# Kernel tuning notes

Hardware: AMD Instinct MI355X
Metric: run time of the kernel (lower is better)

The kernel has to match this reference:

```python
import jax, jax.numpy as jnp
import numpy as np

H = 256
W = 256
CHUNK = 100  # faces per rasterizer scan step


def _cross2(o, p, q):
    # 2D cross product of (p-o) x (q-o); broadcasts over leading dims
    return (p[..., 0] - o[..., 0]) * (q[..., 1] - o[..., 1]) - (p[..., 1] - o[..., 1]) * (q[..., 0] - o[..., 0])


def transform(verts, K, Rt):
    # verts [B,V,3] -> pixel coords [B,V,3] = (x_pix, y_pix, z_cam)
    v_cam = jnp.einsum('bij,bnj->bni', Rt[:, :, :3], verts) + Rt[:, None, :, 3]
    v_proj = jnp.einsum('bij,bnj->bni', K, v_cam)
    z = v_cam[..., 2:3]
    return jnp.concatenate([v_proj[..., :2] / z, z], axis=-1)


def _pixel_centers(h, w, dtype):
    px = jnp.arange(w, dtype=dtype) + 0.5
    py = jnp.arange(h, dtype=dtype) + 0.5
    gx, gy = jnp.meshgrid(px, py, indexing='xy')  # [h,w]
    return gx, gy


def rasterize(v_pix, vi, h, w):
    # z-buffered triangle rasterization -> index image [B,h,w] (int32, -1 = bg)
    B = v_pix.shape[0]
    Fc = vi.shape[0]
    gx, gy = _pixel_centers(h, w, v_pix.dtype)
    pix = jnp.stack([gx.ravel(), gy.ravel()], axis=-1)  # [HW,2]
    face_ids = jnp.arange(Fc, dtype=jnp.int32).reshape(-1, CHUNK)
    inf = jnp.asarray(jnp.inf, v_pix.dtype)

    def step(carry, fids):
        best_z, best_i = carry
        tri = vi[fids]                      # [C,3]
        p = v_pix[:, tri]                   # [B,C,3,3]
        a, b, c = p[:, :, 0], p[:, :, 1], p[:, :, 2]
        area = _cross2(a[..., :2], b[..., :2], c[..., :2])  # [B,C]
        pixb = pix[None, None]              # [1,1,HW,2]
        w0 = _cross2(b[..., None, :2], c[..., None, :2], pixb)  # [B,C,HW]
        w1 = _cross2(c[..., None, :2], a[..., None, :2], pixb)
        w2 = _cross2(a[..., None, :2], b[..., None, :2], pixb)
        s = jnp.sign(area)[..., None]
        nz = jnp.abs(area)[..., None] > 1e-8
        inside = (w0 * s >= 0) & (w1 * s >= 0) & (w2 * s >= 0) & nz
        za, zb, zc = a[..., 2:3], b[..., 2:3], c[..., 2:3]
        valid = inside & (za > 0) & (zb > 0) & (zc > 0)
        ar = jnp.where(jnp.abs(area) > 1e-8, area, 1.0)[..., None]
        invz = (w0 / ar) / za + (w1 / ar) / zb + (w2 / ar) / zc  # persp-correct 1/z
        z = jnp.where(valid & (invz > 0), 1.0 / jnp.maximum(invz, 1e-12), inf)
        cz = z.min(axis=1)                  # [B,HW]
        ci = z.argmin(axis=1)
        cf = fids[ci]
        upd = cz < best_z
        return (jnp.where(upd, cz, best_z), jnp.where(upd, cf, best_i)), None

    init = (jnp.full((B, h * w), jnp.inf, v_pix.dtype), jnp.full((B, h * w), -1, jnp.int32))
    (_, bi), _ = jax.lax.scan(step, init, face_ids)
    return bi.reshape(B, h, w)


def render(v_pix, vi, index_img):
    # depth [B,h,w] and perspective-correct barycentrics [B,3,h,w]
    B, h, w = index_img.shape
    tri = vi[jnp.clip(index_img, 0)]                 # [B,h,w,3]
    p = jax.vmap(lambda v, t: v[t])(v_pix, tri)      # [B,h,w,3,3]
    gx, gy = _pixel_centers(h, w, v_pix.dtype)
    pt = jnp.stack([gx, gy], axis=-1)[None]          # [1,h,w,2]
    a, b, c = p[..., 0, :], p[..., 1, :], p[..., 2, :]
    w0 = _cross2(b[..., :2], c[..., :2], pt)
    w1 = _cross2(c[..., :2], a[..., :2], pt)
    w2 = _cross2(a[..., :2], b[..., :2], pt)
    area = w0 + w1 + w2
    ar = jnp.where(jnp.abs(area) > 1e-8, area, 1.0)
    f0 = (w0 / ar) / jnp.maximum(a[..., 2], 1e-8)
    f1 = (w1 / ar) / jnp.maximum(b[..., 2], 1e-8)
    f2 = (w2 / ar) / jnp.maximum(c[..., 2], 1e-8)
    invz = f0 + f1 + f2
    invz_s = jnp.where(jnp.abs(invz) > 1e-12, invz, 1.0)
    depth = 1.0 / invz_s
    bary = jnp.stack([f0, f1, f2], axis=-1) / invz_s[..., None]  # [B,h,w,3]
    m = index_img != -1
    depth_img = jnp.where(m, depth, 0.0)
    bary_img = jnp.where(m[..., None], bary, 0.0).transpose(0, 3, 1, 2)  # [B,3,h,w]
    return depth_img, bary_img


def interpolate(attr, vti, index_img, bary_img):
    # attr [B,N,D], bary_img [B,3,h,w] -> [B,D,h,w]
    tri = vti[jnp.clip(index_img, 0)]                # [B,h,w,3]
    av = jax.vmap(lambda a, t: a[t])(attr, tri)      # [B,h,w,3,D]
    return jnp.einsum('bhwkd,bkhw->bdhw', av, bary_img)


def grid_sample_bilinear(tex, grid):
    # tex [B,C,Ht,Wt], grid [B,h,w,2] in [-1,1]; align_corners=False, zero pad
    B, C, Ht, Wt = tex.shape
    x = (grid[..., 0] + 1.0) * Wt / 2.0 - 0.5
    y = (grid[..., 1] + 1.0) * Ht / 2.0 - 0.5
    x0 = jnp.floor(x)
    y0 = jnp.floor(y)
    wx = (x - x0)[:, None]
    wy = (y - y0)[:, None]
    x0i = x0.astype(jnp.int32)
    y0i = y0.astype(jnp.int32)

    def gat(ix, iy):
        valid = (ix >= 0) & (ix < Wt) & (iy >= 0) & (iy < Ht)
        ixc = jnp.clip(ix, 0, Wt - 1)
        iyc = jnp.clip(iy, 0, Ht - 1)
        v = jax.vmap(lambda t, yy, xx: t[:, yy, xx])(tex, iyc, ixc)  # [B,C,h,w]
        return v * valid[:, None].astype(tex.dtype)

    return (gat(x0i, y0i) * (1 - wx) * (1 - wy)
            + gat(x0i + 1, y0i) * wx * (1 - wy)
            + gat(x0i, y0i + 1) * (1 - wx) * wy
            + gat(x0i + 1, y0i + 1) * wx * wy)


def reference(verts, tex, K, Rt, vt, vi, vti):
    v_pix = transform(verts, K, Rt)
    index_img = jax.lax.stop_gradient(rasterize(v_pix, vi, H, W))
    depth_img, bary_img = render(v_pix, vi, index_img)
    B = verts.shape[0]
    vt_attr = jnp.broadcast_to((vt * 2.0 - 1.0)[None], (B,) + vt.shape)
    vt_img = interpolate(vt_attr, vti, index_img, bary_img)    # [B,2,H,W]
    mask = (index_img != -1)[:, None].astype(tex.dtype)
    img = grid_sample_bilinear(tex, vt_img.transpose(0, 2, 3, 1)) * mask
    # edge_grad_estimator is identity in the forward pass
    return img, depth_img, v_pix, vt_img, index_img, bary_img, mask


def setup_inputs() -> dict:
    key = jax.random.key(0)
    ks = jax.random.split(key, 6)
    B, V, Fc, Nvt = 2, 5000, 10000, 5000
    xy = jax.random.uniform(ks[0], (B, V, 2), minval=-1.5, maxval=1.5)
    z = jax.random.uniform(ks[1], (B, V, 1), minval=2.0, maxval=4.0)
    verts = jnp.concatenate([xy, z], axis=-1)
    tex = jax.random.uniform(ks[2], (B, 3, 1024, 1024), dtype=jnp.float32)
    K = jnp.broadcast_to(jnp.array([[256., 0., 128.], [0., 256., 128.], [0., 0., 1.]], dtype=jnp.float32), (B, 3, 3))
    Rt = jnp.broadcast_to(jnp.concatenate([jnp.eye(3, dtype=jnp.float32), jnp.zeros((3, 1), jnp.float32)], axis=1), (B, 3, 4))
    vt = jax.random.uniform(ks[3], (Nvt, 2), dtype=jnp.float32)
    vi = jax.random.randint(ks[4], (Fc, 3), 0, V).astype(jnp.int32)
    vti = jax.random.randint(ks[5], (Fc, 3), 0, Nvt).astype(jnp.int32)
    return {"verts": verts, "tex": tex, "K": K, "Rt": Rt, "vt": vt, "vi": vi, "vti": vti}
```

## Files before the change

kernel.cpp:

```cpp
#include <hip/hip_runtime.h>
#include <cmath>

#define H_ 256
#define W_ 256
#define SEG 4
#define NB 256
#define NBAND (H_ / 4)
#define ILV 4
#define REC_STRIDE 24
#define INITKEY 0x7f800000FFFFFFFFull

__device__ inline unsigned fkey(float f) {
  unsigned u = __float_as_uint(f);
  return (u & 0x80000000u) ? ~u : (u | 0x80000000u);
}
__device__ inline float unfkey(unsigned k) {
  return (k & 0x80000000u) ? __uint_as_float(k & 0x7fffffffu) : __uint_as_float(~k);
}

__device__ inline int zbucket(float zmin, float zlo, float scale) {
  int bkt = 0;
  if (zmin == zmin) bkt = min(NB - 1, max(0, (int)((zmin - zlo) * scale)));
  return bkt;
}

__device__ inline bool face_bbox_int(const float* __restrict__ r,
                                     int& xlo, int& xhi, int& ylo, int& yhi) {
  float sp = r[15];
  if (!(sp == sp)) return false;
  float minx = r[17], maxx = r[18], miny = r[19], maxy = r[20];
  int xl = (int)ceilf(fmaxf(fminf(minx - 0.5f, 1e9f), -1e9f));
  int xh = (int)floorf(fmaxf(fminf(maxx - 0.5f, 1e9f), -1e9f));
  int yl = (int)ceilf(fmaxf(fminf(miny - 0.5f, 1e9f), -1e9f));
  int yh = (int)floorf(fmaxf(fminf(maxy - 0.5f, 1e9f), -1e9f));
  if (xl > xh || yl > yh) return false;
  if (xh < 0 || xl > W_ - 1 || yh < 0 || yl > H_ - 1) return false;
  xlo = max(xl, 0); xhi = min(xh, W_ - 1);
  ylo = max(yl, 0); yhi = min(yh, H_ - 1);
  return true;
}

__global__ void k_transform(const float* __restrict__ verts, const float* __restrict__ Km,
                            const float* __restrict__ Rt, float* __restrict__ vpix,
                            int B, int V) {
  int i = blockIdx.x * blockDim.x + threadIdx.x;
  if (i >= B * V) return;
  int b = i / V;
  float x = verts[(size_t)i * 3 + 0], y = verts[(size_t)i * 3 + 1], z = verts[(size_t)i * 3 + 2];
  const float* R = Rt + (size_t)b * 12;
  float cx = __fadd_rn(__fadd_rn(__fadd_rn(__fmul_rn(R[0], x), __fmul_rn(R[1], y)), __fmul_rn(R[2], z)), R[3]);
  float cy = __fadd_rn(__fadd_rn(__fadd_rn(__fmul_rn(R[4], x), __fmul_rn(R[5], y)), __fmul_rn(R[6], z)), R[7]);
  float cz = __fadd_rn(__fadd_rn(__fadd_rn(__fmul_rn(R[8], x), __fmul_rn(R[9], y)), __fmul_rn(R[10], z)), R[11]);
  const float* Kb = Km + (size_t)b * 9;
  float px = __fadd_rn(__fadd_rn(__fmul_rn(Kb[0], cx), __fmul_rn(Kb[1], cy)), __fmul_rn(Kb[2], cz));
  float py = __fadd_rn(__fadd_rn(__fmul_rn(Kb[3], cx), __fmul_rn(Kb[4], cy)), __fmul_rn(Kb[5], cz));
  vpix[(size_t)i * 3 + 0] = __fdiv_rn(px, cz);
  vpix[(size_t)i * 3 + 1] = __fdiv_rn(py, cz);
  vpix[(size_t)i * 3 + 2] = cz;
}

__global__ void k_init(unsigned long long* __restrict__ keys, int nkeys,
                       int* __restrict__ hist, int* __restrict__ cursor, int nbkt,
                       int* __restrict__ cnt, int* __restrict__ bcur, int nband,
                       unsigned* __restrict__ minmax) {
  int i = blockIdx.x * blockDim.x + threadIdx.x;
  if (keys && i < nkeys) keys[i] = INITKEY;
  if (hist && i < nbkt) { hist[i] = 0; cursor[i] = 0; }
  if (cnt && i < nband) { cnt[i] = 0; bcur[i] = 0; }
  if (i == 0 && minmax) { minmax[0] = 0xFFFFFFFFu; minmax[1] = 0u; }
}

__global__ void k_faceprep(const float* __restrict__ vpix, const int* __restrict__ vi,
                           float* __restrict__ rec, unsigned* __restrict__ minmax,
                           int B, int V, int F) {
  int i = blockIdx.x * blockDim.x + threadIdx.x;
  if (i >= B * F) return;
  int b = i / F, f = i - b * F;
  int i0 = vi[f * 3 + 0], i1 = vi[f * 3 + 1], i2 = vi[f * 3 + 2];
  const float* base = vpix + (size_t)b * V * 3;
  float ax = base[(size_t)i0 * 3], ay = base[(size_t)i0 * 3 + 1], az = base[(size_t)i0 * 3 + 2];
  float bx = base[(size_t)i1 * 3], by = base[(size_t)i1 * 3 + 1], bz = base[(size_t)i1 * 3 + 2];
  float cx = base[(size_t)i2 * 3], cy = base[(size_t)i2 * 3 + 1], cz = base[(size_t)i2 * 3 + 2];
  float e0x = __fsub_rn(cx, bx), e0y = __fsub_rn(cy, by);
  float e1x = __fsub_rn(ax, cx), e1y = __fsub_rn(ay, cy);
  float e2x = __fsub_rn(bx, ax), e2y = __fsub_rn(by, ay);
  float area = __fsub_rn(__fmul_rn(e2x, __fsub_rn(cy, ay)), __fmul_rn(e2y, __fsub_rn(cx, ax)));
  float s = (area > 0.f) ? 1.f : ((area < 0.f) ? -1.f : 0.f);
  bool nz = fabsf(area) > 1e-8f;
  bool zv = (az > 0.f) && (bz > 0.f) && (cz > 0.f);
  float sprime = (nz && zv) ? s : __uint_as_float(0x7fc00000u);
  float ar = nz ? area : 1.0f;
  float zmin = fminf(az, fminf(bz, cz));
  float* r = rec + (size_t)i * REC_STRIDE;
  r[0] = ax; r[1] = ay; r[2] = bx; r[3] = by; r[4] = cx; r[5] = cy;
  r[6] = e0x; r[7] = e0y; r[8] = e1x; r[9] = e1y; r[10] = e2x; r[11] = e2y;
  r[12] = az; r[13] = bz; r[14] = cz; r[15] = sprime; r[16] = ar;
  r[17] = fminf(ax, fminf(bx, cx));
  r[18] = fmaxf(ax, fmaxf(bx, cx));
  r[19] = fminf(ay, fminf(by, cy));
  r[20] = fmaxf(ay, fmaxf(by, cy));
  r[21] = zmin; r[22] = 0.f; r[23] = 0.f;
  if (minmax && zmin == zmin) {
    unsigned k = fkey(zmin);
    atomicMin(&minmax[0], k);
    atomicMax(&minmax[1], k);
  }
}

__global__ void k_hist(const float* __restrict__ rec, const unsigned* __restrict__ minmax,
                       int* __restrict__ hist, int* __restrict__ cnt, int B, int F) {
  int i = blockIdx.x * blockDim.x + threadIdx.x;
  if (i >= B * F) return;
  int b = i / F;
  const float* r = rec + (size_t)i * REC_STRIDE;
  float zmin = r[21];
  float zlo = unfkey(minmax[0]), zhi = unfkey(minmax[1]);
  float scale = (float)NB / fmaxf(zhi - zlo, 1e-12f);
  int bkt = zbucket(zmin, zlo, scale);
  atomicAdd(&hist[b * NB + bkt], 1);
  if (cnt) {
    int xlo, xhi, ylo, yhi;
    if (face_bbox_int(r, xlo, xhi, ylo, yhi)) {
      for (int band = (ylo >> 2); band <= (yhi >> 2); ++band)
        atomicAdd(&cnt[(b * NBAND + band) * NB + bkt], 1);
    }
  }
}

__global__ void k_scan(const int* __restrict__ hist, int* __restrict__ boff, int B) {
  __shared__ int sh[NB];
  int t = threadIdx.x;
  for (int b = 0; b < B; ++b) {
    sh[t] = hist[b * NB + t];
    __syncthreads();
    int self = sh[t];
    for (int ofs = 1; ofs < NB; ofs <<= 1) {
      int u = (t >= ofs) ? sh[t - ofs] : 0;
      __syncthreads();
      sh[t] += u;
      __syncthreads();
    }
    boff[b * NB + t] = sh[t] - self;
    __syncthreads();
  }
}

__global__ void k_bandscan(const int* __restrict__ cnt, int* __restrict__ bstart) {
  __shared__ int sh[NB];
  int rowi = blockIdx.x;
  int t = threadIdx.x;
  sh[t] = cnt[rowi * NB + t];
  __syncthreads();
  int self = sh[t];
  for (int ofs = 1; ofs < NB; ofs <<= 1) {
    int u = (t >= ofs) ? sh[t - ofs] : 0;
    __syncthreads();
    sh[t] += u;
    __syncthreads();
  }
  bstart[rowi * (NB + 1) + t] = sh[t] - self;
  if (t == NB - 1) bstart[rowi * (NB + 1) + NB] = sh[t];
}

__global__ void k_scatter(const float* __restrict__ rec, const unsigned* __restrict__ minmax,
                          const int* __restrict__ boff, int* __restrict__ cursor,
                          float4* __restrict__ sA, float4* __restrict__ sB4,
                          float4* __restrict__ sC, float4* __restrict__ sZ1,
                          float4* __restrict__ sbb, float4* __restrict__ sM,
                          const int* __restrict__ bstart, int* __restrict__ bcur,
                          uint4* __restrict__ list, int B, int F) {
  int i = blockIdx.x * blockDim.x + threadIdx.x;
  if (i >= B * F) return;
  int b = i / F, f = i - b * F;
  const float* r = rec + (size_t)i * REC_STRIDE;
  float zmin = r[21];
  float zlo = unfkey(minmax[0]), zhi = unfkey(minmax[1]);
  float rng = fmaxf(zhi - zlo, 1e-12f);
  float scale = (float)NB / rng;
  int bkt = zbucket(zmin, zlo, scale);
  float floorval = zlo + (float)bkt * (rng / (float)NB);
  int pos = boff[b * NB + bkt] + atomicAdd(&cursor[b * NB + bkt], 1);
  size_t gp = (size_t)b * F + pos;
  float sp = r[15];
  sM[gp]  = make_float4(floorval, zmin, __int_as_float(f), 0.f);
  sbb[gp] = make_float4(r[17], r[18], r[19], r[20]);
  sA[gp]  = make_float4(r[0], r[1], r[2], r[3]);
  sB4[gp] = make_float4(r[4], r[5], __fmul_rn(sp, r[6]), __fmul_rn(sp, r[7]));
  sC[gp]  = make_float4(__fmul_rn(sp, r[8]), __fmul_rn(sp, r[9]),
                        __fmul_rn(sp, r[10]), __fmul_rn(sp, r[11]));
  sZ1[gp] = make_float4(r[12], r[13], r[14], __fmul_rn(sp, r[16]));
  if (list) {
    int xlo, xhi, ylo, yhi;
    if (face_bbox_int(r, xlo, xhi, ylo, yhi)) {
      uint4 ent = make_uint4((unsigned)xlo | ((unsigned)xhi << 8) | ((unsigned)ylo << 16) | ((unsigned)yhi << 24),
                             (unsigned)pos | ((unsigned)f << 16),
                             __float_as_uint(zmin), __float_as_uint(floorval));
      for (int band = (ylo >> 2); band <= (yhi >> 2); ++band) {
        int rowi = b * NBAND + band;
        int slot = bstart[rowi * (NB + 1) + bkt] + atomicAdd(&bcur[rowi * NB + bkt], 1);
        list[(size_t)rowi * F + slot] = ent;
      }
    }
  }
}

__global__ __launch_bounds__(64 * ILV) void k_raster_band(const uint4* __restrict__ list,
                                                          const int* __restrict__ bstart,
                                                          const float4* __restrict__ sA,
                                                          const float4* __restrict__ sB4,
                                                          const float4* __restrict__ sC,
                                                          const float4* __restrict__ sZ1,
                                                          float* __restrict__ o_idx,
                                                          int B, int F) {
  int seg = blockIdx.x;
  int y   = blockIdx.y;
  int b   = blockIdx.z;
  int tid = threadIdx.x;
  int w = tid >> 6, lane = tid & 63;
  __shared__ unsigned long long sk[64];
  if (tid < 64) sk[tid] = INITKEY;
  __syncthreads();
  int rowi = b * NBAND + (y >> 2);
  int len = bstart[rowi * (NB + 1) + NB];
  const uint4* L = list + (size_t)rowi * F;
  size_t fb = (size_t)b * F;
  float px = seg * 64 + lane + 0.5f, py = y + 0.5f;
  int sx0 = seg * 64, sx1 = sx0 + 63;
  unsigned long long bestkey = INITKEY;
  float bestz = INFINITY;
  int it = 0;
  int pos = w;
  uint4 e = (pos < len) ? L[pos] : make_uint4(0u, 0u, 0u, 0x7f800000u);
  while (pos < len) {
    int nxt = pos + ILV;
    uint4 en = L[(nxt < len) ? nxt : (len - 1)];
    float floor0 = __fmul_rn(__uint_as_float(e.w), 0.9999f) - 1e-5f;
    if (__all(floor0 > bestz)) break;
    ++it;
    if ((it & 7) == 0) {
      unsigned long long old = atomicMin(&sk[lane], bestkey);
      if (old < bestkey) { bestkey = old; bestz = __uint_as_float((unsigned)(bestkey >> 32)); }
    }
    int xlo = (int)(e.x & 255u), xhi = (int)((e.x >> 8) & 255u);
    int ylo = (int)((e.x >> 16) & 255u), yhi = (int)(e.x >> 24);
    bool cull = (y < ylo) || (y > yhi) || (xhi < sx0) || (xlo > sx1);
    if (!cull) {
      int p = (int)(e.y & 0xffffu);
      float4 a0 = sA[fb + p];
      float4 a1 = sB4[fb + p];
      float4 a2 = sC[fb + p];
      float t0 = __fsub_rn(__fmul_rn(a1.z, __fsub_rn(py, a0.w)), __fmul_rn(a1.w, __fsub_rn(px, a0.z)));
      float t1 = __fsub_rn(__fmul_rn(a2.x, __fsub_rn(py, a1.y)), __fmul_rn(a2.y, __fsub_rn(px, a1.x)));
      float t2 = __fsub_rn(__fmul_rn(a2.z, __fsub_rn(py, a0.y)), __fmul_rn(a2.w, __fsub_rn(px, a0.x)));
      bool inside = (t0 >= 0.f) && (t1 >= 0.f) && (t2 >= 0.f);
      if (inside && !(__fmul_rn(__uint_as_float(e.z), 0.9999f) > bestz)) {
        float4 zz = sZ1[fb + p];
        float u0 = __fdiv_rn(__fdiv_rn(t0, zz.w), zz.x);
        float u1 = __fdiv_rn(__fdiv_rn(t1, zz.w), zz.y);
        float u2 = __fdiv_rn(__fdiv_rn(t2, zz.w), zz.z);
        float invz = __fadd_rn(__fadd_rn(u0, u1), u2);
        if (invz > 0.f) {
          float z = __fdiv_rn(1.0f, fmaxf(invz, 1e-12f));
          unsigned fid = e.y >> 16;
          unsigned long long ck = ((unsigned long long)__float_as_uint(z) << 32) | fid;
          if (ck < bestkey) {
            bestkey = ck; bestz = z;
            atomicMin(&sk[lane], ck);
          }
        }
      }
    }
    pos = nxt;
    e = en;
  }
  atomicMin(&sk[lane], bestkey);
  __syncthreads();
  if (tid < 64) {
    unsigned long long k = sk[tid];
    unsigned zb = (unsigned)(k >> 32);
    o_idx[(size_t)b * (H_ * W_) + (size_t)y * W_ + seg * 64 + tid] =
        (zb >= 0x7f800000u) ? -1.0f : (float)(int)(unsigned)(k & 0xffffffffu);
  }
}

__global__ __launch_bounds__(64 * ILV) void k_raster_tile(const float4* __restrict__ sA,
                                                          const float4* __restrict__ sB4,
                                                          const float4* __restrict__ sC,
                                                          const float4* __restrict__ sZ1,
                                                          const float4* __restrict__ sbb,
                                                          const float4* __restrict__ sM,
                                                          float* __restrict__ o_idx,
                                                          int B, int F) {
  int seg = blockIdx.x;
  int y   = blockIdx.y;
  int b   = blockIdx.z;
  int tid = threadIdx.x;
  int w = tid >> 6, lane = tid & 63;
  __shared__ unsigned long long sk[64];
  if (tid < 64) sk[tid] = INITKEY;
  __syncthreads();
  size_t fb = (size_t)b * F;
  float px = seg * 64 + lane + 0.5f, py = y + 0.5f;
  float wx0 = seg * 64 + 0.5f, wx1 = wx0 + 63.0f;
  unsigned long long bestkey = INITKEY;
  float bestz = INFINITY;
  int it = 0;
  int pos = w;
  float4 M  = sM[fb + pos];
  float4 bb = sbb[fb + pos];
  while (pos < F) {
    int nxt = pos + ILV;
    int nl = (nxt < F) ? nxt : (F - 1);
    float4 Mn  = sM[fb + nl];
    float4 bbn = sbb[fb + nl];
    float floor0 = __fmul_rn(M.x, 0.9999f) - 1e-5f;
    if (__all(floor0 > bestz)) break;
    ++it;
    if ((it & 7) == 0) {
      unsigned long long old = atomicMin(&sk[lane], bestkey);
      if (old < bestkey) { bestkey = old; bestz = __uint_as_float((unsigned)(bestkey >> 32)); }
    }
    bool cull = (py < bb.z) || (py > bb.w) || (bb.y < wx0) || (bb.x > wx1);
    if (!cull) {
      float4 a0 = sA[fb + pos];
      float4 a1 = sB4[fb + pos];
      float4 a2 = sC[fb + pos];
      float t0 = __fsub_rn(__fmul_rn(a1.z, __fsub_rn(py, a0.w)), __fmul_rn(a1.w, __fsub_rn(px, a0.z)));
      float t1 = __fsub_rn(__fmul_rn(a2.x, __fsub_rn(py, a1.y)), __fmul_rn(a2.y, __fsub_rn(px, a1.x)));
      float t2 = __fsub_rn(__fmul_rn(a2.z, __fsub_rn(py, a0.y)), __fmul_rn(a2.w, __fsub_rn(px, a0.x)));
      bool inside = (t0 >= 0.f) && (t1 >= 0.f) && (t2 >= 0.f);
      if (inside && !(__fmul_rn(M.y, 0.9999f) > bestz)) {
        float4 zz = sZ1[fb + pos];
        float u0 = __fdiv_rn(__fdiv_rn(t0, zz.w), zz.x);
        float u1 = __fdiv_rn(__fdiv_rn(t1, zz.w), zz.y);
        float u2 = __fdiv_rn(__fdiv_rn(t2, zz.w), zz.z);
        float invz = __fadd_rn(__fadd_rn(u0, u1), u2);
        if (invz > 0.f) {
          float z = __fdiv_rn(1.0f, fmaxf(invz, 1e-12f));
          int fid = __float_as_int(M.z);
          unsigned long long ck = ((unsigned long long)__float_as_uint(z) << 32) | (unsigned)fid;
          if (ck < bestkey) { bestkey = ck; bestz = z; atomicMin(&sk[lane], ck); }
        }
      }
    }
    pos = nxt;
    M = Mn; bb = bbn;
  }
  atomicMin(&sk[lane], bestkey);
  __syncthreads();
  if (tid < 64) {
    unsigned long long k = sk[tid];
    unsigned zb = (unsigned)(k >> 32);
    o_idx[(size_t)b * (H_ * W_) + (size_t)y * W_ + seg * 64 + tid] =
        (zb >= 0x7f800000u) ? -1.0f : (float)(int)(unsigned)(k & 0xffffffffu);
  }
}

__global__ void k_raster_direct(const float* __restrict__ vpix, const int* __restrict__ vi,
                                float* __restrict__ idxout, int B, int V, int F) {
  int p = blockIdx.x * blockDim.x + threadIdx.x;
  if (p >= B * H_ * W_) return;
  int b = p / (H_ * W_); int pid = p - b * (H_ * W_);
  float px = (pid & (W_ - 1)) + 0.5f, py = (pid >> 8) + 0.5f;
  const float* base = vpix + (size_t)b * V * 3;
  float bestz = INFINITY; int besti = -1;
  for (int f = 0; f < F; ++f) {
    int i0 = vi[f * 3], i1 = vi[f * 3 + 1], i2 = vi[f * 3 + 2];
    float ax = base[(size_t)i0 * 3], ay = base[(size_t)i0 * 3 + 1], za = base[(size_t)i0 * 3 + 2];
    float bx = base[(size_t)i1 * 3], by = base[(size_t)i1 * 3 + 1], zb = base[(size_t)i1 * 3 + 2];
    float cx = base[(size_t)i2 * 3], cy = base[(size_t)i2 * 3 + 1], zc = base[(size_t)i2 * 3 + 2];
    float e0x = __fsub_rn(cx, bx), e0y = __fsub_rn(cy, by);
    float e1x = __fsub_rn(ax, cx), e1y = __fsub_rn(ay, cy);
    float e2x = __fsub_rn(bx, ax), e2y = __fsub_rn(by, ay);
    float area = __fsub_rn(__fmul_rn(e2x, __fsub_rn(cy, ay)), __fmul_rn(e2y, __fsub_rn(cx, ax)));
    float s = (area > 0.f) ? 1.f : ((area < 0.f) ? -1.f : 0.f);
    bool nz = fabsf(area) > 1e-8f;
    bool zv = (za > 0.f) && (zb > 0.f) && (zc > 0.f);
    float sp = (nz && zv) ? s : __uint_as_float(0x7fc00000u);
    float ar = nz ? area : 1.0f;
    float w0 = __fsub_rn(__fmul_rn(e0x, __fsub_rn(py, by)), __fmul_rn(e0y, __fsub_rn(px, bx)));
    float w1 = __fsub_rn(__fmul_rn(e1x, __fsub_rn(py, cy)), __fmul_rn(e1y, __fsub_rn(px, cx)));
    float w2 = __fsub_rn(__fmul_rn(e2x, __fsub_rn(py, ay)), __fmul_rn(e2y, __fsub_rn(px, ax)));
    bool inside = (__fmul_rn(w0, sp) >= 0.f) && (__fmul_rn(w1, sp) >= 0.f) && (__fmul_rn(w2, sp) >= 0.f);
    if (inside) {
      float invz = __fadd_rn(__fadd_rn(__fdiv_rn(__fdiv_rn(w0, ar), za),
                                       __fdiv_rn(__fdiv_rn(w1, ar), zb)),
                             __fdiv_rn(__fdiv_rn(w2, ar), zc));
      if (invz > 0.f) {
        float z = __fdiv_rn(1.0f, fmaxf(invz, 1e-12f));
        if (z < bestz) { bestz = z; besti = f; }
      }
    }
  }
  idxout[p] = (float)besti;
}

__global__ __launch_bounds__(256) void k_render(const float* __restrict__ vpix, const int* __restrict__ vi,
                                                const int* __restrict__ vti, const float* __restrict__ vt,
                                                const float* __restrict__ tex, const float* __restrict__ idxin,
                                                float* __restrict__ o_img, float* __restrict__ o_depth,
                                                float* __restrict__ o_vt, float* __restrict__ o_bary,
                                                float* __restrict__ o_mask,
                                                int B, int V, int F, int TH, int TW) {
  int p = blockIdx.x * blockDim.x + threadIdx.x;
  if (p >= B * H_ * W_) return;
  int HW = H_ * W_;
  int b = p / HW; int pid = p - b * HW;
  int y = pid >> 8, x = pid & (W_ - 1);
  int idx = (int)idxin[p];
  size_t pix2 = (size_t)b * 2 * HW + pid;
  size_t pix3 = (size_t)b * 3 * HW + pid;
  if (idx < 0) {
    o_depth[p] = 0.f; o_mask[p] = 0.f;
    o_vt[pix2] = 0.f; o_vt[pix2 + HW] = 0.f;
    o_bary[pix3] = 0.f; o_bary[pix3 + HW] = 0.f; o_bary[pix3 + 2 * HW] = 0.f;
    o_img[pix3] = 0.f; o_img[pix3 + HW] = 0.f; o_img[pix3 + 2 * HW] = 0.f;
    return;
  }
  const float* base = vpix + (size_t)b * V * 3;
  int i0 = vi[idx * 3], i1 = vi[idx * 3 + 1], i2 = vi[idx * 3 + 2];
  float ax = base[(size_t)i0 * 3], ay = base[(size_t)i0 * 3 + 1], az = base[(size_t)i0 * 3 + 2];
  float bx = base[(size_t)i1 * 3], by = base[(size_t)i1 * 3 + 1], bz = base[(size_t)i1 * 3 + 2];
  float cx = base[(size_t)i2 * 3], cy = base[(size_t)i2 * 3 + 1], cz = base[(size_t)i2 * 3 + 2];
  float ptx = x + 0.5f, pty = y + 0.5f;
  float w0 = __fsub_rn(__fmul_rn(__fsub_rn(cx, bx), __fsub_rn(pty, by)),
                       __fmul_rn(__fsub_rn(cy, by), __fsub_rn(ptx, bx)));
  float w1 = __fsub_rn(__fmul_rn(__fsub_rn(ax, cx), __fsub_rn(pty, cy)),
                       __fmul_rn(__fsub_rn(ay, cy), __fsub_rn(ptx, cx)));
  float w2 = __fsub_rn(__fmul_rn(__fsub_rn(bx, ax), __fsub_rn(pty, ay)),
                       __fmul_rn(__fsub_rn(by, ay), __fsub_rn(ptx, ax)));
  float area = __fadd_rn(__fadd_rn(w0, w1), w2);
  float ar = (fabsf(area) > 1e-8f) ? area : 1.0f;
  float f0 = __fdiv_rn(__fdiv_rn(w0, ar), fmaxf(az, 1e-8f));
  float f1 = __fdiv_rn(__fdiv_rn(w1, ar), fmaxf(bz, 1e-8f));
  float f2 = __fdiv_rn(__fdiv_rn(w2, ar), fmaxf(cz, 1e-8f));
  float invz = __fadd_rn(__fadd_rn(f0, f1), f2);
  float invz_s = (fabsf(invz) > 1e-12f) ? invz : 1.0f;
  float depth = __fdiv_rn(1.0f, invz_s);
  float bary0 = __fdiv_rn(f0, invz_s);
  float bary1 = __fdiv_rn(f1, invz_s);
  float bary2 = __fdiv_rn(f2, invz_s);
  o_depth[p] = depth; o_mask[p] = 1.0f;
  o_bary[pix3] = bary0; o_bary[pix3 + HW] = bary1; o_bary[pix3 + 2 * HW] = bary2;
  int t0 = vti[idx * 3], t1 = vti[idx * 3 + 1], t2 = vti[idx * 3 + 2];
  float u0x = __fsub_rn(__fmul_rn(vt[(size_t)t0 * 2], 2.f), 1.f);
  float u0y = __fsub_rn(__fmul_rn(vt[(size_t)t0 * 2 + 1], 2.f), 1.f);
  float u1x = __fsub_rn(__fmul_rn(vt[(size_t)t1 * 2], 2.f), 1.f);
  float u1y = __fsub_rn(__fmul_rn(vt[(size_t)t1 * 2 + 1], 2.f), 1.f);
  float u2x = __fsub_rn(__fmul_rn(vt[(size_t)t2 * 2], 2.f), 1.f);
  float u2y = __fsub_rn(__fmul_rn(vt[(size_t)t2 * 2 + 1], 2.f), 1.f);
  float gx = __fadd_rn(__fadd_rn(__fmul_rn(u0x, bary0), __fmul_rn(u1x, bary1)), __fmul_rn(u2x, bary2));
  float gy = __fadd_rn(__fadd_rn(__fmul_rn(u0y, bary0), __fmul_rn(u1y, bary1)), __fmul_rn(u2y, bary2));
  o_vt[pix2] = gx; o_vt[pix2 + HW] = gy;
  float sx = __fsub_rn(__fdiv_rn(__fmul_rn(__fadd_rn(gx, 1.0f), (float)TW), 2.0f), 0.5f);
  float sy = __fsub_rn(__fdiv_rn(__fmul_rn(__fadd_rn(gy, 1.0f), (float)TH), 2.0f), 0.5f);
  float x0f = floorf(sx), y0f = floorf(sy);
  float wx = __fsub_rn(sx, x0f), wy = __fsub_rn(sy, y0f);
  float omx = __fsub_rn(1.0f, wx), omy = __fsub_rn(1.0f, wy);
  int x0 = (int)x0f, y0 = (int)y0f;
  int x1 = x0 + 1, y1 = y0 + 1;
  bool v00 = (x0 >= 0) && (x0 < TW) && (y0 >= 0) && (y0 < TH);
  bool v10 = (x1 >= 0) && (x1 < TW) && (y0 >= 0) && (y0 < TH);
  bool v01 = (x0 >= 0) && (x0 < TW) && (y1 >= 0) && (y1 < TH);
  bool v11 = (x1 >= 0) && (x1 < TW) && (y1 >= 0) && (y1 < TH);
  int x0c = min(max(x0, 0), TW - 1), x1c = min(max(x1, 0), TW - 1);
  int y0c = min(max(y0, 0), TH - 1), y1c = min(max(y1, 0), TH - 1);
  const float* tb = tex + (size_t)b * 3 * TH * TW;
  #pragma unroll
  for (int ch = 0; ch < 3; ++ch) {
    const float* tc = tb + (size_t)ch * TH * TW;
    float g00 = v00 ? tc[(size_t)y0c * TW + x0c] : 0.f;
    float g10 = v10 ? tc[(size_t)y0c * TW + x1c] : 0.f;
    float g01 = v01 ? tc[(size_t)y1c * TW + x0c] : 0.f;
    float g11 = v11 ? tc[(size_t)y1c * TW + x1c] : 0.f;
    float r = __fmul_rn(__fmul_rn(g00, omx), omy);
    r = __fadd_rn(r, __fmul_rn(__fmul_rn(g10, wx), omy));
    r = __fadd_rn(r, __fmul_rn(__fmul_rn(g01, omx), wy));
    r = __fadd_rn(r, __fmul_rn(__fmul_rn(g11, wx), wy));
    o_img[pix3 + (size_t)ch * HW] = r;
  }
}

extern "C" void kernel_launch(void* const* d_in, const int* in_sizes, int n_in,
                              void* d_out, int out_size, void* d_ws, size_t ws_size,
                              hipStream_t stream) {
  const float* verts = (const float*)d_in[0];
  const float* tex   = (const float*)d_in[1];
  const float* Km    = (const float*)d_in[2];
  const float* Rt    = (const float*)d_in[3];
  const float* vt    = (const float*)d_in[4];
  const int*   vi    = (const int*)d_in[5];
  const int*   vti   = (const int*)d_in[6];

  int B = in_sizes[2] / 9;
  int V = in_sizes[0] / (3 * B);
  int F = in_sizes[5] / 3;
  long texhw = (long)in_sizes[1] / (B * 3);
  int TH = (int)(sqrt((double)texhw) + 0.5);
  int TW = TH;
  const int HW = H_ * W_;

  float* out = (float*)d_out;
  float* o_img   = out;
  float* o_depth = o_img + (size_t)B * 3 * HW;
  float* o_vpix  = o_depth + (size_t)B * HW;
  float* o_vt    = o_vpix + (size_t)B * V * 3;
  float* o_idx   = o_vt + (size_t)B * 2 * HW;
  float* o_bary  = o_idx + (size_t)B * HW;
  float* o_mask  = o_bary + (size_t)B * 3 * HW;

  k_transform<<<(B * V + 255) / 256, 256, 0, stream>>>(verts, Km, Rt, o_vpix, B, V);

  size_t f4Bytes    = (size_t)B * F * 16;
  size_t recBytes   = (size_t)B * F * REC_STRIDE * 4;
  size_t histBytes  = (size_t)B * NB * 4;
  size_t listBytes  = (size_t)B * NBAND * F * 16;
  size_t cntBytes   = (size_t)B * NBAND * NB * 4;
  size_t bstBytes   = (size_t)B * NBAND * (NB + 1) * 4;
  size_t keysBytes  = (size_t)B * HW * 8;
  size_t needBinned = 6 * f4Bytes + listBytes + recBytes + 3 * histBytes +
                      2 * cntBytes + bstBytes + 64;
  size_t needSorted = 6 * f4Bytes + recBytes + 3 * histBytes + 16;
  size_t needBasic  = keysBytes + recBytes;

  if (ws_size >= needSorted) {
    bool binned = (ws_size >= needBinned) && (F <= 65535);
    char* w = (char*)d_ws;
    float4* sA  = (float4*)w;  w += f4Bytes;
    float4* sB4 = (float4*)w;  w += f4Bytes;
    float4* sC  = (float4*)w;  w += f4Bytes;
    float4* sZ1 = (float4*)w;  w += f4Bytes;
    float4* sbb = (float4*)w;  w += f4Bytes;
    float4* sM  = (float4*)w;  w += f4Bytes;
    uint4*  list = nullptr;
    if (binned) { list = (uint4*)w; w += listBytes; }
    float*  rec = (float*)w;   w += recBytes;
    int*    hist = (int*)w;    w += histBytes;
    int*    boff = (int*)w;    w += histBytes;
    int*    cursor = (int*)w;  w += histBytes;
    int *cnt = nullptr, *bstart = nullptr, *bcur = nullptr;
    if (binned) {
      cnt = (int*)w;    w += cntBytes;
      bcur = (int*)w;   w += cntBytes;
      bstart = (int*)w; w += bstBytes;
    }
    unsigned* minmax = (unsigned*)w;

    int ninit = binned ? (B * NBAND * NB) : (B * NB);
    k_init<<<(ninit + 255) / 256, 256, 0, stream>>>((unsigned long long*)nullptr, 0,
                                                    hist, cursor, B * NB,
                                                    cnt, bcur, binned ? B * NBAND * NB : 0, minmax);
    k_faceprep<<<(B * F + 255) / 256, 256, 0, stream>>>(o_vpix, vi, rec, minmax, B, V, F);
    k_hist<<<(B * F + 255) / 256, 256, 0, stream>>>(rec, minmax, hist, cnt, B, F);
    k_scan<<<1, NB, 0, stream>>>(hist, boff, B);
    if (binned) k_bandscan<<<B * NBAND, NB, 0, stream>>>(cnt, bstart);
    k_scatter<<<(B * F + 255) / 256, 256, 0, stream>>>(rec, minmax, boff, cursor,
                                                       sA, sB4, sC, sZ1, sbb, sM,
                                                       bstart, bcur, list, B, F);
    dim3 rg(W_ / 64, H_, B);
    if (binned)
      k_raster_band<<<rg, 64 * ILV, 0, stream>>>(list, bstart, sA, sB4, sC, sZ1, o_idx, B, F);
    else
      k_raster_tile<<<rg, 64 * ILV, 0, stream>>>(sA, sB4, sC, sZ1, sbb, sM, o_idx, B, F);
  } else {
    k_raster_direct<<<(B * HW + 255) / 256, 256, 0, stream>>>(o_vpix, vi, o_idx, B, V, F);
  }

  k_render<<<(B * HW + 255) / 256, 256, 0, stream>>>(o_vpix, vi, vti, vt, tex, o_idx,
                                                     o_img, o_depth, o_vt, o_bary, o_mask,
                                                     B, V, F, TH, TW);
}
```

Before: 415.7 us.

## Embed edge coefficients in band list entries and deepen prefetch pipeline

Each band list entry grows from 16 to 64 bytes and now carries the edge-function coefficients inline, so the raster loop no longer does dependent gathers into sA/sB4/sC. Band height changes from 4 to 16 rows, which gives fewer bands, less duplication and fewer scatter atomics. The loop prefetches two entries ahead and reads per-entry metadata with readfirstlane. The cost is a list four times larger, more scatter write traffic and longer per-band lists that rows must scan.

```diff
diff --git a/kernel.cpp b/kernel.cpp
--- a/kernel.cpp
+++ b/kernel.cpp
@@ -3,9 +3,9 @@
 
 #define H_ 256
 #define W_ 256
-#define SEG 4
 #define NB 256
-#define NBAND (H_ / 4)
+#define BANDSH 4
+#define NBAND (H_ >> BANDSH)
 #define ILV 4
 #define REC_STRIDE 24
 #define INITKEY 0x7f800000FFFFFFFFull
@@ -59,12 +59,10 @@
   vpix[(size_t)i * 3 + 2] = cz;
 }
 
-__global__ void k_init(unsigned long long* __restrict__ keys, int nkeys,
-                       int* __restrict__ hist, int* __restrict__ cursor, int nbkt,
+__global__ void k_init(int* __restrict__ hist, int* __restrict__ cursor, int nbkt,
                        int* __restrict__ cnt, int* __restrict__ bcur, int nband,
                        unsigned* __restrict__ minmax) {
   int i = blockIdx.x * blockDim.x + threadIdx.x;
-  if (keys && i < nkeys) keys[i] = INITKEY;
   if (hist && i < nbkt) { hist[i] = 0; cursor[i] = 0; }
   if (cnt && i < nband) { cnt[i] = 0; bcur[i] = 0; }
   if (i == 0 && minmax) { minmax[0] = 0xFFFFFFFFu; minmax[1] = 0u; }
@@ -121,7 +119,7 @@
   if (cnt) {
     int xlo, xhi, ylo, yhi;
     if (face_bbox_int(r, xlo, xhi, ylo, yhi)) {
-      for (int band = (ylo >> 2); band <= (yhi >> 2); ++band)
+      for (int band = (ylo >> BANDSH); band <= (yhi >> BANDSH); ++band)
         atomicAdd(&cnt[(b * NBAND + band) * NB + bkt], 1);
     }
   }
@@ -182,23 +180,30 @@
   int pos = boff[b * NB + bkt] + atomicAdd(&cursor[b * NB + bkt], 1);
   size_t gp = (size_t)b * F + pos;
   float sp = r[15];
+  float4 a0 = make_float4(r[0], r[1], r[2], r[3]);
+  float4 a1 = make_float4(r[4], r[5], __fmul_rn(sp, r[6]), __fmul_rn(sp, r[7]));
+  float4 a2 = make_float4(__fmul_rn(sp, r[8]), __fmul_rn(sp, r[9]),
+                          __fmul_rn(sp, r[10]), __fmul_rn(sp, r[11]));
   sM[gp]  = make_float4(floorval, zmin, __int_as_float(f), 0.f);
   sbb[gp] = make_float4(r[17], r[18], r[19], r[20]);
-  sA[gp]  = make_float4(r[0], r[1], r[2], r[3]);
-  sB4[gp] = make_float4(r[4], r[5], __fmul_rn(sp, r[6]), __fmul_rn(sp, r[7]));
-  sC[gp]  = make_float4(__fmul_rn(sp, r[8]), __fmul_rn(sp, r[9]),
-                        __fmul_rn(sp, r[10]), __fmul_rn(sp, r[11]));
+  sA[gp]  = a0;
+  sB4[gp] = a1;
+  sC[gp]  = a2;
   sZ1[gp] = make_float4(r[12], r[13], r[14], __fmul_rn(sp, r[16]));
   if (list) {
     int xlo, xhi, ylo, yhi;
     if (face_bbox_int(r, xlo, xhi, ylo, yhi)) {
-      uint4 ent = make_uint4((unsigned)xlo | ((unsigned)xhi << 8) | ((unsigned)ylo << 16) | ((unsigned)yhi << 24),
-                             (unsigned)pos | ((unsigned)f << 16),
-                             __float_as_uint(zmin), __float_as_uint(floorval));
-      for (int band = (ylo >> 2); band <= (yhi >> 2); ++band) {
+      uint4 meta = make_uint4((unsigned)xlo | ((unsigned)xhi << 8) | ((unsigned)ylo << 16) | ((unsigned)yhi << 24),
+                              (unsigned)pos | ((unsigned)f << 16),
+                              __float_as_uint(zmin), __float_as_uint(floorval));
+      uint4 u1 = make_uint4(__float_as_uint(a0.x), __float_as_uint(a0.y), __float_as_uint(a0.z), __float_as_uint(a0.w));
+      uint4 u2 = make_uint4(__float_as_uint(a1.x), __float_as_uint(a1.y), __float_as_uint(a1.z), __float_as_uint(a1.w));
+      uint4 u3 = make_uint4(__float_as_uint(a2.x), __float_as_uint(a2.y), __float_as_uint(a2.z), __float_as_uint(a2.w));
+      for (int band = (ylo >> BANDSH); band <= (yhi >> BANDSH); ++band) {
         int rowi = b * NBAND + band;
         int slot = bstart[rowi * (NB + 1) + bkt] + atomicAdd(&bcur[rowi * NB + bkt], 1);
-        list[(size_t)rowi * F + slot] = ent;
+        uint4* eb = list + ((size_t)rowi * F + slot) * 4;
+        eb[0] = meta; eb[1] = u1; eb[2] = u2; eb[3] = u3;
       }
     }
   }
@@ -206,9 +211,6 @@
 
 __global__ __launch_bounds__(64 * ILV) void k_raster_band(const uint4* __restrict__ list,
                                                           const int* __restrict__ bstart,
-                                                          const float4* __restrict__ sA,
-                                                          const float4* __restrict__ sB4,
-                                                          const float4* __restrict__ sC,
                                                           const float4* __restrict__ sZ1,
                                                           float* __restrict__ o_idx,
                                                           int B, int F) {
@@ -220,59 +222,77 @@
   __shared__ unsigned long long sk[64];
   if (tid < 64) sk[tid] = INITKEY;
   __syncthreads();
-  int rowi = b * NBAND + (y >> 2);
+  int rowi = b * NBAND + (y >> BANDSH);
   int len = bstart[rowi * (NB + 1) + NB];
-  const uint4* L = list + (size_t)rowi * F;
+  const uint4* Lr = list + (size_t)rowi * F * 4;
   size_t fb = (size_t)b * F;
   float px = seg * 64 + lane + 0.5f, py = y + 0.5f;
   int sx0 = seg * 64, sx1 = sx0 + 63;
   unsigned long long bestkey = INITKEY;
   float bestz = INFINITY;
-  int it = 0;
-  int pos = w;
-  uint4 e = (pos < len) ? L[pos] : make_uint4(0u, 0u, 0u, 0x7f800000u);
-  while (pos < len) {
-    int nxt = pos + ILV;
-    uint4 en = L[(nxt < len) ? nxt : (len - 1)];
-    float floor0 = __fmul_rn(__uint_as_float(e.w), 0.9999f) - 1e-5f;
-    if (__all(floor0 > bestz)) break;
-    ++it;
-    if ((it & 7) == 0) {
-      unsigned long long old = atomicMin(&sk[lane], bestkey);
-      if (old < bestkey) { bestkey = old; bestz = __uint_as_float((unsigned)(bestkey >> 32)); }
-    }
-    int xlo = (int)(e.x & 255u), xhi = (int)((e.x >> 8) & 255u);
-    int ylo = (int)((e.x >> 16) & 255u), yhi = (int)(e.x >> 24);
-    bool cull = (y < ylo) || (y > yhi) || (xhi < sx0) || (xlo > sx1);
-    if (!cull) {
-      int p = (int)(e.y & 0xffffu);
-      float4 a0 = sA[fb + p];
-      float4 a1 = sB4[fb + p];
-      float4 a2 = sC[fb + p];
-      float t0 = __fsub_rn(__fmul_rn(a1.z, __fsub_rn(py, a0.w)), __fmul_rn(a1.w, __fsub_rn(px, a0.z)));
-      float t1 = __fsub_rn(__fmul_rn(a2.x, __fsub_rn(py, a1.y)), __fmul_rn(a2.y, __fsub_rn(px, a1.x)));
-      float t2 = __fsub_rn(__fmul_rn(a2.z, __fsub_rn(py, a0.y)), __fmul_rn(a2.w, __fsub_rn(px, a0.x)));
-      bool inside = (t0 >= 0.f) && (t1 >= 0.f) && (t2 >= 0.f);
-      if (inside && !(__fmul_rn(__uint_as_float(e.z), 0.9999f) > bestz)) {
-        float4 zz = sZ1[fb + p];
-        float u0 = __fdiv_rn(__fdiv_rn(t0, zz.w), zz.x);
-        float u1 = __fdiv_rn(__fdiv_rn(t1, zz.w), zz.y);
-        float u2 = __fdiv_rn(__fdiv_rn(t2, zz.w), zz.z);
-        float invz = __fadd_rn(__fadd_rn(u0, u1), u2);
-        if (invz > 0.f) {
-          float z = __fdiv_rn(1.0f, fmaxf(invz, 1e-12f));
-          unsigned fid = e.y >> 16;
-          unsigned long long ck = ((unsigned long long)__float_as_uint(z) << 32) | fid;
-          if (ck < bestkey) {
-            bestkey = ck; bestz = z;
-            atomicMin(&sk[lane], ck);
+  unsigned long long out;
+  if (len <= 0) goto done;
+  {
+    uint4 A0, A1, A2, A3, B0, B1, B2, B3;
+    int pos = w;
+    {
+      int q0 = (pos < len) ? pos : (len - 1);
+      const uint4* e = Lr + (size_t)q0 * 4;
+      A0 = e[0]; A1 = e[1]; A2 = e[2]; A3 = e[3];
+      int q1 = (pos + ILV < len) ? (pos + ILV) : (len - 1);
+      e = Lr + (size_t)q1 * 4;
+      B0 = e[0]; B1 = e[1]; B2 = e[2]; B3 = e[3];
+    }
+    int it = 0;
+    while (pos < len) {
+      int q2 = (pos + 2 * ILV < len) ? (pos + 2 * ILV) : (len - 1);
+      const uint4* e2 = Lr + (size_t)q2 * 4;
+      uint4 C0 = e2[0], C1 = e2[1], C2 = e2[2], C3 = e2[3];
+      unsigned bbox = __builtin_amdgcn_readfirstlane(A0.x);
+      unsigned pfid = __builtin_amdgcn_readfirstlane(A0.y);
+      float zmn = __uint_as_float(__builtin_amdgcn_readfirstlane(A0.z));
+      float zfl = __uint_as_float(__builtin_amdgcn_readfirstlane(A0.w));
+      float floor0 = __fmul_rn(zfl, 0.9999f) - 1e-5f;
+      if (__all(floor0 > bestz)) break;
+      ++it;
+      if ((it & 7) == 0) {
+        unsigned long long old = atomicMin(&sk[lane], bestkey);
+        if (old < bestkey) { bestkey = old; bestz = __uint_as_float((unsigned)(bestkey >> 32)); }
+      }
+      int xlo = (int)(bbox & 255u), xhi = (int)((bbox >> 8) & 255u);
+      int ylo = (int)((bbox >> 16) & 255u), yhi = (int)(bbox >> 24);
+      if (!((y < ylo) || (y > yhi) || (xhi < sx0) || (xlo > sx1))) {
+        float4 a0 = make_float4(__uint_as_float(A1.x), __uint_as_float(A1.y), __uint_as_float(A1.z), __uint_as_float(A1.w));
+        float4 a1 = make_float4(__uint_as_float(A2.x), __uint_as_float(A2.y), __uint_as_float(A2.z), __uint_as_float(A2.w));
+        float4 a2 = make_float4(__uint_as_float(A3.x), __uint_as_float(A3.y), __uint_as_float(A3.z), __uint_as_float(A3.w));
+        float t0 = __fsub_rn(__fmul_rn(a1.z, __fsub_rn(py, a0.w)), __fmul_rn(a1.w, __fsub_rn(px, a0.z)));
+        float t1 = __fsub_rn(__fmul_rn(a2.x, __fsub_rn(py, a1.y)), __fmul_rn(a2.y, __fsub_rn(px, a1.x)));
+        float t2 = __fsub_rn(__fmul_rn(a2.z, __fsub_rn(py, a0.y)), __fmul_rn(a2.w, __fsub_rn(px, a0.x)));
+        bool inside = (t0 >= 0.f) && (t1 >= 0.f) && (t2 >= 0.f);
+        if (inside && !(__fmul_rn(zmn, 0.9999f) > bestz)) {
+          int p = (int)(pfid & 0xffffu);
+          float4 zz = sZ1[fb + p];
+          float u0 = __fdiv_rn(__fdiv_rn(t0, zz.w), zz.x);
+          float u1 = __fdiv_rn(__fdiv_rn(t1, zz.w), zz.y);
+          float u2 = __fdiv_rn(__fdiv_rn(t2, zz.w), zz.z);
+          float invz = __fadd_rn(__fadd_rn(u0, u1), u2);
+          if (invz > 0.f) {
+            float z = __fdiv_rn(1.0f, fmaxf(invz, 1e-12f));
+            unsigned fid = pfid >> 16;
+            unsigned long long ck = ((unsigned long long)__float_as_uint(z) << 32) | fid;
+            if (ck < bestkey) {
+              bestkey = ck; bestz = z;
+              atomicMin(&sk[lane], ck);
+            }
           }
         }
       }
-    }
-    pos = nxt;
-    e = en;
-  }
+      pos += ILV;
+      A0 = B0; A1 = B1; A2 = B2; A3 = B3;
+      B0 = C0; B1 = C1; B2 = C2; B3 = C3;
+    }
+  }
+done:
   atomicMin(&sk[lane], bestkey);
   __syncthreads();
   if (tid < 64) {
@@ -281,6 +301,7 @@
     o_idx[(size_t)b * (H_ * W_) + (size_t)y * W_ + seg * 64 + tid] =
         (zb >= 0x7f800000u) ? -1.0f : (float)(int)(unsigned)(k & 0xffffffffu);
   }
+  (void)out;
 }
 
 __global__ __launch_bounds__(64 * ILV) void k_raster_tile(const float4* __restrict__ sA,
@@ -514,14 +535,12 @@
   size_t f4Bytes    = (size_t)B * F * 16;
   size_t recBytes   = (size_t)B * F * REC_STRIDE * 4;
   size_t histBytes  = (size_t)B * NB * 4;
-  size_t listBytes  = (size_t)B * NBAND * F * 16;
+  size_t listBytes  = (size_t)B * NBAND * F * 64;
   size_t cntBytes   = (size_t)B * NBAND * NB * 4;
   size_t bstBytes   = (size_t)B * NBAND * (NB + 1) * 4;
-  size_t keysBytes  = (size_t)B * HW * 8;
   size_t needBinned = 6 * f4Bytes + listBytes + recBytes + 3 * histBytes +
                       2 * cntBytes + bstBytes + 64;
   size_t needSorted = 6 * f4Bytes + recBytes + 3 * histBytes + 16;
-  size_t needBasic  = keysBytes + recBytes;
 
   if (ws_size >= needSorted) {
     bool binned = (ws_size >= needBinned) && (F <= 65535);
@@ -547,8 +566,7 @@
     unsigned* minmax = (unsigned*)w;
 
     int ninit = binned ? (B * NBAND * NB) : (B * NB);
-    k_init<<<(ninit + 255) / 256, 256, 0, stream>>>((unsigned long long*)nullptr, 0,
-                                                    hist, cursor, B * NB,
+    k_init<<<(ninit + 255) / 256, 256, 0, stream>>>(hist, cursor, B * NB,
                                                     cnt, bcur, binned ? B * NBAND * NB : 0, minmax);
     k_faceprep<<<(B * F + 255) / 256, 256, 0, stream>>>(o_vpix, vi, rec, minmax, B, V, F);
     k_hist<<<(B * F + 255) / 256, 256, 0, stream>>>(rec, minmax, hist, cnt, B, F);
@@ -559,7 +577,7 @@
                                                        bstart, bcur, list, B, F);
     dim3 rg(W_ / 64, H_, B);
     if (binned)
-      k_raster_band<<<rg, 64 * ILV, 0, stream>>>(list, bstart, sA, sB4, sC, sZ1, o_idx, B, F);
+      k_raster_band<<<rg, 64 * ILV, 0, stream>>>(list, bstart, sZ1, o_idx, B, F);
     else
       k_raster_tile<<<rg, 64 * ILV, 0, stream>>>(sA, sB4, sC, sZ1, sbb, sM, o_idx, B, F);
   } else {
```

Result: no change. 412.9 us (-0.7%).
